# Performance work log

Measured on AMD Instinct MI355X. Metric: run time of the kernel, lower is better.

Reference implementation:

```python
import jax, jax.numpy as jnp
import numpy as np

NC = 6            # CPAB tessellation cells (tess_size=6, zero_boundary=True)
DIM = NC - 1      # theta dimension = 5
SIG_LEN = 2048
CHANNELS = 3
BATCH = 256
FC_IN = 64 * 168  # flattened net_part1 output for signal_len=2048
NUM_SCALING = 0   # N in transform_data_ss
EPS_BN = 1e-5


def _cpab_basis():
    """QR null-space basis of the CPAB continuity + zero-boundary constraints.
    Params ordered [a_1,b_1,...,a_NC,b_NC]; v(x)=a_c x + b_c on cell c."""
    nc = NC
    L = np.zeros((nc + 1, 2 * nc))
    for k in range(1, nc):  # continuity at internal knots x_k = k/nc
        xk = k / nc
        L[k - 1, 2 * (k - 1)] = xk
        L[k - 1, 2 * (k - 1) + 1] = 1.0
        L[k - 1, 2 * k] = -xk
        L[k - 1, 2 * k + 1] = -1.0
    L[nc - 1, 1] = 1.0        # v(0) = 0  -> b_1 = 0
    L[nc, 2 * (nc - 1)] = 1.0  # v(1) = 0 -> a_nc + b_nc = 0
    L[nc, 2 * nc - 1] = 1.0
    Q, _ = np.linalg.qr(L.T, mode='complete')
    return np.ascontiguousarray(Q[:, nc + 1:]).astype(np.float32)  # (12, 5)


def _conv1d(x, w, b):
    y = jax.lax.conv_general_dilated(x, w, (1,), 'VALID',
                                     dimension_numbers=('NCH', 'OIH', 'NCH'))
    return y + b[None, :, None]


def _maxpool1d(x, k, s):
    return jax.lax.reduce_window(x, -jnp.inf, jax.lax.max, (1, 1, k), (1, 1, s), 'VALID')


def _bn(x, g, b, m, v):  # eval-mode BatchNorm1d
    return (x - m[None, :, None]) * (g / jnp.sqrt(v + EPS_BN))[None, :, None] + b[None, :, None]


def _integrate(x, A):
    """Exact CPAB 1D flow integration over t=1 with cell-crossing handling.
    x: (B, n) points in [0,1]; A: (B, NC, 2) per-cell (a, b). Monotone
    trajectories cross at most NC-1 boundaries -> fixed NC+1 iterations."""
    a_all, b_all = A[:, :, 0], A[:, :, 1]
    t = jnp.ones_like(x)
    for _ in range(NC + 1):
        c = jnp.clip(jnp.floor(x * NC).astype(jnp.int32), 0, NC - 1)
        a = jnp.take_along_axis(a_all, c, axis=1)
        b = jnp.take_along_axis(b_all, c, axis=1)
        v = a * x + b
        xb = jnp.where(v >= 0, (c + 1).astype(x.dtype) / NC, c.astype(x.dtype) / NC)
        big_a = jnp.abs(a) > 1e-8
        a_s = jnp.where(big_a, a, 1.0)
        z = x + b / a_s        # shifted coord: x(t) = z*exp(a t) - b/a
        zb = xb + b / a_s
        ratio = zb / jnp.where(jnp.abs(z) > 1e-12, z, 1e-12)
        t_exp = jnp.log(jnp.maximum(ratio, 1e-12)) / a_s
        v_s = jnp.where(jnp.abs(v) > 1e-12, v, 1.0)
        t_lin = (xb - x) / v_s
        thit = jnp.where(big_a, t_exp, t_lin)
        valid = (jnp.abs(v) > 1e-12) & (thit > 0) & (jnp.where(big_a, ratio, 1.0) > 0)
        thit = jnp.where(valid, thit, jnp.inf)
        tau = jnp.minimum(t, thit)
        x_new = jnp.where(big_a, z * jnp.exp(a * tau) - (z - x), x + b * tau)
        hit = thit <= t
        nudge = jnp.where(v >= 0, 1e-6, -1e-6)  # push into next cell
        x = jnp.clip(jnp.where(hit, xb + nudge, x_new), 0.0, 1.0)
        t = jnp.maximum(t - tau, 0.0)
    return x


def _interp1d(data, pos):
    """data: (B, L, C); pos: (B, n) in [0,1] -> (B, n, C) linear interpolation."""
    Lw = data.shape[1]
    p = jnp.clip(pos, 0.0, 1.0) * (Lw - 1)
    x0 = jnp.clip(jnp.floor(p).astype(jnp.int32), 0, Lw - 2)
    w = (p - x0.astype(p.dtype))[:, :, None]
    d0 = jnp.take_along_axis(data, x0[:, :, None], axis=1)
    d1 = jnp.take_along_axis(data, (x0 + 1)[:, :, None], axis=1)
    return d0 * (1.0 - w) + d1 * w


def _transform_data_ss(data, theta, basis, outsize, N):
    """CPAB scaling-and-squaring warp of data (B, L, C) by theta (B, DIM)."""
    Bsz = theta.shape[0]
    A = (theta @ basis.T).reshape(Bsz, NC, 2) / (2.0 ** N)
    grid = jnp.linspace(0.0, 1.0, outsize, dtype=data.dtype)
    grid_t = _integrate(jnp.broadcast_to(grid, (Bsz, outsize)), A)
    for _ in range(N):  # squaring: compose the warp with itself
        grid_t = _interp1d(grid_t[:, :, None], grid_t)[:, :, 0]
    return _interp1d(data, grid_t)


def reference(x, conv1_w, conv1_b, bn1_g, bn1_b, bn1_m, bn1_v,
              conv2_w, conv2_b, bn2_g, bn2_b, bn2_m, bn2_v,
              conv3_w, conv3_b, bn3_g, bn3_b, bn3_m, bn3_v,
              fc1_w, fc1_b, fc2_w, fc2_b, fc3_w, fc3_b, fc4_w, fc4_b, basis):
    # localization net (n_recurrence = 1, back_version = True)
    h = jax.nn.relu(_maxpool1d(_bn(_conv1d(x, conv1_w, conv1_b), bn1_g, bn1_b, bn1_m, bn1_v), 3, 2))
    h = jax.nn.relu(_maxpool1d(_bn(_conv1d(h, conv2_w, conv2_b), bn2_g, bn2_b, bn2_m, bn2_v), 3, 3))
    h = jax.nn.relu(_maxpool1d(_bn(_conv1d(h, conv3_w, conv3_b), bn3_g, bn3_b, bn3_m, bn3_v), 3, 2))
    xs = h.reshape(h.shape[0], -1)  # (B, 64*168)
    xs = jax.nn.relu(xs @ fc1_w.T + fc1_b)
    xs = jax.nn.relu(xs @ fc2_w.T + fc2_b)
    xs = jax.nn.relu(xs @ fc3_w.T + fc3_b)
    theta = jnp.tanh(xs @ fc4_w.T + fc4_b)  # (B, 5)
    data = jnp.transpose(x, (0, 2, 1))       # (B, L, C)
    warped = _transform_data_ss(data, theta, basis, SIG_LEN, NUM_SCALING)
    return jnp.transpose(warped, (0, 2, 1))  # (B, C, L)


def setup_inputs() -> dict:
    key = jax.random.key(0)
    ks = jax.random.split(key, 16)
    def nrm(k, shape, scale):
        return (jax.random.normal(k, shape) * scale).astype(jnp.float32)
    inp = {}
    inp['x'] = jax.random.normal(ks[0], (BATCH, CHANNELS, SIG_LEN), dtype=jnp.float32)
    inp['conv1_w'] = nrm(ks[1], (128, CHANNELS, 3), (CHANNELS * 3) ** -0.5)
    inp['conv1_b'] = nrm(ks[2], (128,), 0.01)
    inp['bn1_g'] = jnp.ones((128,), jnp.float32)
    inp['bn1_b'] = jnp.zeros((128,), jnp.float32)
    inp['bn1_m'] = nrm(ks[3], (128,), 0.1)
    inp['bn1_v'] = jnp.ones((128,), jnp.float32)
    inp['conv2_w'] = nrm(ks[4], (64, 128, 5), (128 * 5) ** -0.5)
    inp['conv2_b'] = nrm(ks[5], (64,), 0.01)
    inp['bn2_g'] = jnp.ones((64,), jnp.float32)
    inp['bn2_b'] = jnp.zeros((64,), jnp.float32)
    inp['bn2_m'] = nrm(ks[6], (64,), 0.1)
    inp['bn2_v'] = jnp.ones((64,), jnp.float32)
    inp['conv3_w'] = nrm(ks[7], (64, 64, 3), (64 * 3) ** -0.5)
    inp['conv3_b'] = nrm(ks[8], (64,), 0.01)
    inp['bn3_g'] = jnp.ones((64,), jnp.float32)
    inp['bn3_b'] = jnp.zeros((64,), jnp.float32)
    inp['bn3_m'] = nrm(ks[9], (64,), 0.1)
    inp['bn3_v'] = jnp.ones((64,), jnp.float32)
    inp['fc1_w'] = nrm(ks[10], (48, FC_IN), FC_IN ** -0.5)
    inp['fc1_b'] = jnp.zeros((48,), jnp.float32)
    inp['fc2_w'] = nrm(ks[11], (32, 48), 48 ** -0.5)
    inp['fc2_b'] = jnp.zeros((32,), jnp.float32)
    inp['fc3_w'] = nrm(ks[12], (16, 32), 32 ** -0.5)
    inp['fc3_b'] = jnp.zeros((16,), jnp.float32)
    # near-identity warp head (original zero-inits weight, identity bias)
    inp['fc4_w'] = nrm(ks[13], (DIM, 16), 0.01)
    inp['fc4_b'] = nrm(ks[14], (DIM,), 0.01)
    inp['basis'] = jnp.asarray(_cpab_basis())
    return inp
```

## Files before the change

kernel.cpp:

```cpp
#include <hip/hip_runtime.h>
#include <math.h>

#define BATCH   256
#define SIGLEN  2048
#define L1OUT   1022
#define L2OUT   339
#define L3OUT   168
#define FCIN    10752

#define TP2   16
#define NROW  52
#define H1S   136
#define H1SZ  (NROW*H1S)

#define TU3   28

typedef float f32x4  __attribute__((ext_vector_type(4)));
typedef short s16x8  __attribute__((ext_vector_type(8)));

__device__ __forceinline__ unsigned short f2bf(float f) {
    unsigned int u = __float_as_uint(f);
    return (unsigned short)((u + 0x7fffu + ((u >> 16) & 1u)) >> 16);
}
__device__ __forceinline__ float bf2f(unsigned short h) {
    return __uint_as_float(((unsigned int)h) << 16);
}

__launch_bounds__(256)
__global__ void prep_kernel(
    const float* __restrict__ conv1_b,
    const float* __restrict__ g1, const float* __restrict__ b1,
    const float* __restrict__ m1, const float* __restrict__ v1,
    const float* __restrict__ conv2_w, const float* __restrict__ conv2_b,
    const float* __restrict__ g2, const float* __restrict__ b2,
    const float* __restrict__ m2, const float* __restrict__ v2,
    const float* __restrict__ conv3_w, const float* __restrict__ conv3_b,
    const float* __restrict__ g3, const float* __restrict__ b3,
    const float* __restrict__ m3, const float* __restrict__ v3,
    const float* __restrict__ fc1_w,
    unsigned short* __restrict__ w2hi, unsigned short* __restrict__ w2lo,
    unsigned short* __restrict__ w3hi, unsigned short* __restrict__ w3lo,
    float* __restrict__ wp1,
    float* __restrict__ so1, float* __restrict__ so2, float* __restrict__ so3)
{
    __shared__ float tl[64 * 169];

    int t   = threadIdx.x;
    int tid = blockIdx.x * 256 + t;
    int stride = gridDim.x * 256;

    if (blockIdx.x < 48) {
        int o = blockIdx.x;
        for (int i = t; i < FCIN; i += 256) {
            int co = i / L3OUT, u = i - co * L3OUT;
            tl[co * 169 + u] = fc1_w[o * FCIN + i];
        }
        __syncthreads();
        for (int i = t; i < FCIN; i += 256) {
            int u = i >> 6, co = i & 63;
            wp1[o * FCIN + i] = tl[co * 169 + u];
        }
    }

    for (int i = tid; i < 64*128*5; i += stride) {
        int co = i / 640; int rr = i - co*640; int ci = rr / 5; int k = rr - ci*5;
        float w = conv2_w[i];
        unsigned short hi = f2bf(w);
        unsigned short lo = f2bf(w - bf2f(hi));
        int dst = ((k*4 + (ci >> 5))*64 + co)*32 + (ci & 31);
        w2hi[dst] = hi;
        w2lo[dst] = lo;
    }
    for (int i = tid; i < 64*64*3; i += stride) {
        int co = i / 192; int r = i - co*192; int ci = r / 3; int k = r - ci*3;
        float w = conv3_w[i];
        unsigned short hi = f2bf(w);
        unsigned short lo = f2bf(w - bf2f(hi));
        int dst = ((k*2 + (ci >> 5))*64 + co)*32 + (ci & 31);
        w3hi[dst] = hi;
        w3lo[dst] = lo;
    }
    if (tid < 128) {
        float s = g1[tid] / sqrtf(v1[tid] + 1e-5f);
        so1[tid]       = s;
        so1[128 + tid] = (conv1_b[tid] - m1[tid]) * s + b1[tid];
    }
    if (tid < 64) {
        float s2 = g2[tid] / sqrtf(v2[tid] + 1e-5f);
        so2[tid]      = s2;
        so2[64 + tid] = (conv2_b[tid] - m2[tid]) * s2 + b2[tid];
        float s3 = g3[tid] / sqrtf(v3[tid] + 1e-5f);
        so3[tid]      = s3;
        so3[64 + tid] = (conv3_b[tid] - m3[tid]) * s3 + b3[tid];
    }
}

__launch_bounds__(256, 5)
__global__ void conv12_kernel(
    const float* __restrict__ x, const float* __restrict__ w1,
    const unsigned short* __restrict__ w2hi, const unsigned short* __restrict__ w2lo,
    const float* __restrict__ so1, const float* __restrict__ so2,
    unsigned int* __restrict__ h2p)
{
    __shared__ unsigned short h1hi[H1SZ];
    __shared__ unsigned short h1lo[H1SZ];

    int t  = threadIdx.x;
    int b  = blockIdx.x;
    int u0 = blockIdx.y * TP2;
    int q0 = 3 * u0;
    int wv = __builtin_amdgcn_readfirstlane(t >> 6);
    int l  = t & 63;
    int m  = l & 15;
    int qd = l >> 4;

    float wr[2][9];
    float s1r[2], o1r[2];
    #pragma unroll
    for (int h = 0; h < 2; ++h) {
        int ch = l + 64*h;
        #pragma unroll
        for (int j = 0; j < 9; ++j) wr[h][j] = w1[ch*9 + j];
        s1r[h] = so1[ch]; o1r[h] = so1[128 + ch];
    }
    for (int s = 0; s < 13; ++s) {
        int r = 4*s + wv;
        int xbase = 2*(q0 + r);
        float xv[3][5];
        if (xbase + 4 <= SIGLEN - 1) {
            #pragma unroll
            for (int ci = 0; ci < 3; ++ci) {
                const float* xp = x + (b*3 + ci)*SIGLEN + xbase;
                float2 v01 = *(const float2*)(xp);
                float2 v23 = *(const float2*)(xp + 2);
                xv[ci][0] = v01.x; xv[ci][1] = v01.y;
                xv[ci][2] = v23.x; xv[ci][3] = v23.y;
                xv[ci][4] = xp[4];
            }
        } else {
            #pragma unroll
            for (int ci = 0; ci < 3; ++ci) {
                const float* xp = x + (b*3 + ci)*SIGLEN;
                #pragma unroll
                for (int d = 0; d < 5; ++d) {
                    int xi = xbase + d; xi = xi < SIGLEN ? xi : SIGLEN - 1;
                    xv[ci][d] = xp[xi];
                }
            }
        }
        #pragma unroll
        for (int h = 0; h < 2; ++h) {
            float r0 = 0.f, r1 = 0.f, r2 = 0.f;
            #pragma unroll
            for (int ci = 0; ci < 3; ++ci) {
                float wA = wr[h][ci*3], wB = wr[h][ci*3+1], wC = wr[h][ci*3+2];
                r0 = fmaf(xv[ci][0], wA, fmaf(xv[ci][1], wB, fmaf(xv[ci][2], wC, r0)));
                r1 = fmaf(xv[ci][1], wA, fmaf(xv[ci][2], wB, fmaf(xv[ci][3], wC, r1)));
                r2 = fmaf(xv[ci][2], wA, fmaf(xv[ci][3], wB, fmaf(xv[ci][4], wC, r2)));
            }
            float mx = fmaxf(r0, fmaxf(r1, r2));
            float v  = fmaxf(fmaf(s1r[h], mx, o1r[h]), 0.f);
            unsigned short hi = f2bf(v);
            unsigned short lo = f2bf(v - bf2f(hi));
            h1hi[r*H1S + l + 64*h] = hi;
            h1lo[r*H1S + l + 64*h] = lo;
        }
    }
    __syncthreads();

    f32x4 acc[3] = {(f32x4)(0.f), (f32x4)(0.f), (f32x4)(0.f)};

    const unsigned short* whb = w2hi + wv*512 + m*32 + qd*8;
    const unsigned short* wlb = w2lo + wv*512 + m*32 + qd*8;

    for (int k = 0; k < 5; ++k) {
        #pragma unroll
        for (int cb = 0; cb < 4; ++cb) {
            int st = k*4 + cb;
            s16x8 wh = *(const s16x8*)(whb + st*2048);
            s16x8 wl = *(const s16x8*)(wlb + st*2048);
            #pragma unroll
            for (int pt = 0; pt < 3; ++pt) {
                int row = pt*16 + m + k;
                s16x8 ah = *(const s16x8*)&h1hi[row*H1S + cb*32 + qd*8];
                s16x8 al = *(const s16x8*)&h1lo[row*H1S + cb*32 + qd*8];
                acc[pt] = __builtin_amdgcn_mfma_f32_16x16x32_bf16(ah, wh, acc[pt], 0, 0, 0);
                acc[pt] = __builtin_amdgcn_mfma_f32_16x16x32_bf16(al, wh, acc[pt], 0, 0, 0);
                acc[pt] = __builtin_amdgcn_mfma_f32_16x16x32_bf16(ah, wl, acc[pt], 0, 0, 0);
            }
        }
    }
    __syncthreads();

    float* c2 = (float*)h1hi;
    #pragma unroll
    for (int pt = 0; pt < 3; ++pt)
        #pragma unroll
        for (int rg = 0; rg < 4; ++rg)
            c2[(pt*16 + qd*4 + rg)*65 + wv*16 + m] = acc[pt][rg];
    __syncthreads();

    #pragma unroll
    for (int it = 0; it < 4; ++it) {
        int idx = t + it*256;
        int ul = idx >> 6, co = idx & 63;
        int u = u0 + ul;
        if (u < L2OUT) {
            float v0 = c2[(3*ul  )*65 + co];
            float v1 = c2[(3*ul+1)*65 + co];
            float v2 = c2[(3*ul+2)*65 + co];
            float mm = fmaxf(v0, fmaxf(v1, v2));
            float v  = fmaxf(fmaf(so2[co], mm, so2[64 + co]), 0.f);
            unsigned short hi = f2bf(v);
            unsigned short lo = f2bf(v - bf2f(hi));
            h2p[(b*L2OUT + u)*64 + co] = (unsigned int)hi | ((unsigned int)lo << 16);
        }
    }
}

__launch_bounds__(256, 4)
__global__ void conv3fc1_kernel(
    const unsigned int* __restrict__ h2p,
    const unsigned short* __restrict__ w3hi, const unsigned short* __restrict__ w3lo,
    const float* __restrict__ so3, const float* __restrict__ wp1,
    float* __restrict__ part)
{
    __shared__ unsigned short h3s[2*66*72];
    __shared__ float c3buf[64*65];

    int t  = threadIdx.x;
    int b  = blockIdx.x;
    int ti = blockIdx.y;
    int u0 = ti * TU3;
    int wv = __builtin_amdgcn_readfirstlane(t >> 6);
    int l  = t & 63;
    int m  = l & 15;
    int qd = l >> 4;

    for (int i = t; i < 66*64; i += 256) {
        int r = i >> 6, ci = i & 63;
        int g = 2*u0 + r; g = g > (L2OUT-1) ? (L2OUT-1) : g;
        unsigned int v = h2p[(b*L2OUT + g)*64 + ci];
        h3s[r*72 + ci]         = (unsigned short)(v & 0xffffu);
        h3s[66*72 + r*72 + ci] = (unsigned short)(v >> 16);
    }
    __syncthreads();

    s16x8 wh[6], wl[6];
    #pragma unroll
    for (int s = 0; s < 6; ++s) {
        wh[s] = *(const s16x8*)(w3hi + s*2048 + (wv*16 + m)*32 + qd*8);
        wl[s] = *(const s16x8*)(w3lo + s*2048 + (wv*16 + m)*32 + qd*8);
    }

    f32x4 acc[4] = {(f32x4)(0.f), (f32x4)(0.f), (f32x4)(0.f), (f32x4)(0.f)};
    #pragma unroll
    for (int pt = 0; pt < 4; ++pt) {
        #pragma unroll
        for (int s = 0; s < 6; ++s) {
            int row = pt*16 + m + (s >> 1);
            int off = (s & 1)*32 + qd*8;
            s16x8 ah = *(const s16x8*)&h3s[row*72 + off];
            s16x8 al = *(const s16x8*)&h3s[66*72 + row*72 + off];
            acc[pt] = __builtin_amdgcn_mfma_f32_16x16x32_bf16(ah, wh[s], acc[pt], 0, 0, 0);
            acc[pt] = __builtin_amdgcn_mfma_f32_16x16x32_bf16(al, wh[s], acc[pt], 0, 0, 0);
            acc[pt] = __builtin_amdgcn_mfma_f32_16x16x32_bf16(ah, wl[s], acc[pt], 0, 0, 0);
        }
    }
    __syncthreads();

    #pragma unroll
    for (int pt = 0; pt < 4; ++pt)
        #pragma unroll
        for (int rg = 0; rg < 4; ++rg)
            c3buf[(pt*16 + qd*4 + rg)*65 + wv*16 + m] = acc[pt][rg];
    __syncthreads();

    float s3 = so3[l], o3 = so3[64 + l];
    float pooled[TU3];
    #pragma unroll
    for (int u = 0; u < TU3; ++u) {
        int p = 2*u;
        float v0 = c3buf[(p  )*65 + l];
        float v1 = c3buf[(p+1)*65 + l];
        float v2 = c3buf[(p+2)*65 + l];
        pooled[u] = fmaxf(fmaf(s3, fmaxf(v0, fmaxf(v1, v2)), o3), 0.f);
    }

    int o0 = wv * 12;
    float fa[12];
    #pragma unroll
    for (int j = 0; j < 12; ++j) fa[j] = 0.f;
    #pragma unroll 4
    for (int u = 0; u < TU3; ++u) {
        float pv = pooled[u];
        const float* wp = wp1 + (u0 + u)*64 + l;
        #pragma unroll
        for (int j = 0; j < 12; ++j)
            fa[j] = fmaf(pv, wp[(o0 + j)*FCIN], fa[j]);
    }
    #pragma unroll
    for (int j = 0; j < 12; ++j) {
        #pragma unroll
        for (int off = 32; off > 0; off >>= 1)
            fa[j] += __shfl_xor(fa[j], off, 64);
    }
    if (l == 0) {
        #pragma unroll
        for (int j = 0; j < 12; ++j)
            part[(b*6 + ti)*48 + o0 + j] = fa[j];
    }
}

__launch_bounds__(256)
__global__ void warp_kernel(
    const float* __restrict__ x, const float* __restrict__ part,
    const float* __restrict__ fc1_b,
    const float* __restrict__ fc2_w, const float* __restrict__ fc2_b,
    const float* __restrict__ fc3_w, const float* __restrict__ fc3_b,
    const float* __restrict__ fc4_w, const float* __restrict__ fc4_b,
    const float* __restrict__ basis,
    float* __restrict__ out)
{
    __shared__ float xs48[48], hl[32], gl[16], thl[5], Al[12];

    int b = blockIdx.x;
    int t = threadIdx.x;

    if (t < 48) {
        float sv = 0.f;
        #pragma unroll
        for (int ti = 0; ti < 6; ++ti) sv += part[(b*6 + ti)*48 + t];
        xs48[t] = fmaxf(sv + fc1_b[t], 0.f);
    }
    __syncthreads();
    if (t < 32) {
        float sv = fc2_b[t];
        #pragma unroll
        for (int k = 0; k < 48; ++k) sv = fmaf(fc2_w[t * 48 + k], xs48[k], sv);
        hl[t] = fmaxf(sv, 0.f);
    }
    __syncthreads();
    if (t < 16) {
        float sv = fc3_b[t];
        #pragma unroll
        for (int k = 0; k < 32; ++k) sv = fmaf(fc3_w[t * 32 + k], hl[k], sv);
        gl[t] = fmaxf(sv, 0.f);
    }
    __syncthreads();
    if (t < 5) {
        float sv = fc4_b[t];
        #pragma unroll
        for (int k = 0; k < 16; ++k) sv = fmaf(fc4_w[t * 16 + k], gl[k], sv);
        thl[t] = tanhf(sv);
    }
    __syncthreads();
    if (t < 12) {
        float sv = 0.f;
        #pragma unroll
        for (int d = 0; d < 5; ++d) sv = fmaf(basis[t * 5 + d], thl[d], sv);
        Al[t] = sv;
    }
    __syncthreads();

    float a_r[6], b_r[6];
    #pragma unroll
    for (int c = 0; c < 6; ++c) { a_r[c] = Al[2*c]; b_r[c] = Al[2*c+1]; }

    #pragma unroll
    for (int cc = 0; cc < 2; ++cc) {
        int i = (blockIdx.y * 2 + cc) * 256 + t;
        float xp = (float)i / 2047.f;
        float tt = 1.f;
        for (int it = 0; it < 7; ++it) {
            int c = (int)floorf(xp * 6.f);
            c = min(max(c, 0), 5);
            float a  = a_r[c], bb = b_r[c];
            float v  = a * xp + bb;
            float xb = (v >= 0.f) ? (float)(c + 1) / 6.f : (float)c / 6.f;
            bool  big_a = fabsf(a) > 1e-8f;
            float a_s = big_a ? a : 1.f;
            float z   = xp + bb / a_s;
            float zb  = xb + bb / a_s;
            float zden = (fabsf(z) > 1e-12f) ? z : 1e-12f;
            float ratio = zb / zden;
            float t_exp = logf(fmaxf(ratio, 1e-12f)) / a_s;
            float v_s   = (fabsf(v) > 1e-12f) ? v : 1.f;
            float t_lin = (xb - xp) / v_s;
            float thit  = big_a ? t_exp : t_lin;
            bool valid  = (fabsf(v) > 1e-12f) && (thit > 0.f) && ((big_a ? ratio : 1.f) > 0.f);
            if (!valid) thit = __builtin_inff();
            float tau   = fminf(tt, thit);
            float x_new = big_a ? (z * expf(a * tau) - (z - xp)) : (xp + bb * tau);
            bool hit    = (thit <= tt);
            float nudge = (v >= 0.f) ? 1e-6f : -1e-6f;
            xp = hit ? (xb + nudge) : x_new;
            xp = fminf(fmaxf(xp, 0.f), 1.f);
            tt = fmaxf(tt - tau, 0.f);
        }
        float p = fminf(fmaxf(xp, 0.f), 1.f) * 2047.f;
        int i0 = (int)floorf(p);
        i0 = min(max(i0, 0), 2046);
        float w = p - (float)i0;
        #pragma unroll
        for (int c = 0; c < 3; ++c) {
            const float* d = &x[(b * 3 + c) * SIGLEN];
            out[(b * 3 + c) * SIGLEN + i] = d[i0] * (1.f - w) + d[i0 + 1] * w;
        }
    }
}

extern "C" void kernel_launch(void* const* d_in, const int* in_sizes, int n_in,
                              void* d_out, int out_size, void* d_ws, size_t ws_size,
                              hipStream_t stream) {
    (void)in_sizes; (void)n_in; (void)out_size; (void)ws_size;
    const float* x       = (const float*)d_in[0];
    const float* conv1_w = (const float*)d_in[1];
    const float* conv1_b = (const float*)d_in[2];
    const float* bn1_g   = (const float*)d_in[3];
    const float* bn1_b   = (const float*)d_in[4];
    const float* bn1_m   = (const float*)d_in[5];
    const float* bn1_v   = (const float*)d_in[6];
    const float* conv2_w = (const float*)d_in[7];
    const float* conv2_b = (const float*)d_in[8];
    const float* bn2_g   = (const float*)d_in[9];
    const float* bn2_b   = (const float*)d_in[10];
    const float* bn2_m   = (const float*)d_in[11];
    const float* bn2_v   = (const float*)d_in[12];
    const float* conv3_w = (const float*)d_in[13];
    const float* conv3_b = (const float*)d_in[14];
    const float* bn3_g   = (const float*)d_in[15];
    const float* bn3_b   = (const float*)d_in[16];
    const float* bn3_m   = (const float*)d_in[17];
    const float* bn3_v   = (const float*)d_in[18];
    const float* fc1_w   = (const float*)d_in[19];
    const float* fc1_b   = (const float*)d_in[20];
    const float* fc2_w   = (const float*)d_in[21];
    const float* fc2_b   = (const float*)d_in[22];
    const float* fc3_w   = (const float*)d_in[23];
    const float* fc3_b   = (const float*)d_in[24];
    const float* fc4_w   = (const float*)d_in[25];
    const float* fc4_b   = (const float*)d_in[26];
    const float* basis   = (const float*)d_in[27];

    unsigned short* w2hi = (unsigned short*)d_ws;
    unsigned short* w2lo = w2hi + 40960;
    unsigned short* w3hi = w2lo + 40960;
    unsigned short* w3lo = w3hi + 12288;
    float* ws   = (float*)d_ws;
    float* so1  = ws + 53248;
    float* so2  = so1 + 256;
    float* so3  = so2 + 128;
    float* wp1  = so3 + 128;
    unsigned int* h2p = (unsigned int*)(wp1 + 516096);
    float* part = (float*)(h2p + 5554176);

    prep_kernel<<<128, 256, 0, stream>>>(
        conv1_b, bn1_g, bn1_b, bn1_m, bn1_v,
        conv2_w, conv2_b, bn2_g, bn2_b, bn2_m, bn2_v,
        conv3_w, conv3_b, bn3_g, bn3_b, bn3_m, bn3_v,
        fc1_w, w2hi, w2lo, w3hi, w3lo, wp1, so1, so2, so3);

    dim3 g2(BATCH, (L2OUT + TP2 - 1) / TP2);
    conv12_kernel<<<g2, 256, 0, stream>>>(x, conv1_w, w2hi, w2lo, so1, so2, h2p);

    dim3 g3(BATCH, 6);
    conv3fc1_kernel<<<g3, 256, 0, stream>>>(h2p, w3hi, w3lo, so3, wp1, part);

    dim3 g5(BATCH, 4);
    warp_kernel<<<g5, 256, 0, stream>>>(x, part, fc1_b, fc2_w, fc2_b,
                                        fc3_w, fc3_b, fc4_w, fc4_b, basis,
                                        (float*)d_out);
}
```

Baseline: 247.4 us.

## Restructure conv12 with 32x32 MFMA tiles, larger blocks, swizzled LDS and sliding-window conv1

Doubles the conv2 output tile per block to 32 pooled positions with 512 threads, and switches the conv2 GEMM from 16x16x32 to 32x32x16 bf16 MFMA with a matching weight layout. The block has 8 waves but only 6 run MFMA tiles, and which waves sit idle rotates with the block index. Conv1 now uses a per-wave sliding window that reuses the overlapping window result and loads only two new inputs per row. h1 is stored as packed channel pairs with an XOR swizzle to avoid LDS bank conflicts. The bf16 hi/lo split now uses truncation instead of round-to-nearest, which changes rounding slightly. The larger tile wastes some rows at the sequence tail, and the bigger LDS footprint may reduce occupancy.

After: 250.0 us. About the same (+1.0%).

```diff
diff --git a/kernel.cpp b/kernel.cpp
--- a/kernel.cpp
+++ b/kernel.cpp
@@ -8,15 +8,15 @@
 #define L3OUT   168
 #define FCIN    10752
 
-#define TP2   16
-#define NROW  52
-#define H1S   136
-#define H1SZ  (NROW*H1S)
+#define TP2   32
+#define NROW  100
+#define PLANE (NROW*128)
 
 #define TU3   28
 
-typedef float f32x4  __attribute__((ext_vector_type(4)));
-typedef short s16x8  __attribute__((ext_vector_type(8)));
+typedef float f32x4   __attribute__((ext_vector_type(4)));
+typedef float f32x16  __attribute__((ext_vector_type(16)));
+typedef short s16x8   __attribute__((ext_vector_type(8)));
 
 __device__ __forceinline__ unsigned short f2bf(float f) {
     unsigned int u = __float_as_uint(f);
@@ -67,7 +67,7 @@
         float w = conv2_w[i];
         unsigned short hi = f2bf(w);
         unsigned short lo = f2bf(w - bf2f(hi));
-        int dst = ((k*4 + (ci >> 5))*64 + co)*32 + (ci & 31);
+        int dst = ((k*8 + (ci >> 4))*64 + co)*16 + (ci & 15);
         w2hi[dst] = hi;
         w2lo[dst] = lo;
     }
@@ -95,114 +95,172 @@
     }
 }
 
-__launch_bounds__(256, 5)
+__launch_bounds__(512, 6)
 __global__ void conv12_kernel(
     const float* __restrict__ x, const float* __restrict__ w1,
     const unsigned short* __restrict__ w2hi, const unsigned short* __restrict__ w2lo,
     const float* __restrict__ so1, const float* __restrict__ so2,
     unsigned int* __restrict__ h2p)
 {
-    __shared__ unsigned short h1hi[H1SZ];
-    __shared__ unsigned short h1lo[H1SZ];
+    __shared__ unsigned short h1[2*PLANE];
+    unsigned short* h1hi = h1;
+    unsigned short* h1lo = h1 + PLANE;
 
     int t  = threadIdx.x;
     int b  = blockIdx.x;
-    int u0 = blockIdx.y * TP2;
-    int q0 = 3 * u0;
+    int by = blockIdx.y;
+    int u0 = by * TP2;
     int wv = __builtin_amdgcn_readfirstlane(t >> 6);
     int l  = t & 63;
-    int m  = l & 15;
-    int qd = l >> 4;
-
-    float wr[2][9];
-    float s1r[2], o1r[2];
-    #pragma unroll
-    for (int h = 0; h < 2; ++h) {
-        int ch = l + 64*h;
-        #pragma unroll
-        for (int j = 0; j < 9; ++j) wr[h][j] = w1[ch*9 + j];
-        s1r[h] = so1[ch]; o1r[h] = so1[128 + ch];
-    }
-    for (int s = 0; s < 13; ++s) {
-        int r = 4*s + wv;
-        int xbase = 2*(q0 + r);
-        float xv[3][5];
-        if (xbase + 4 <= SIGLEN - 1) {
+
+    {
+        float wr[2][9], s1r[2], o1r[2];
+        #pragma unroll
+        for (int h = 0; h < 2; ++h) {
+            int ch = 2*l + h;
+            #pragma unroll
+            for (int j = 0; j < 9; ++j) wr[h][j] = w1[ch*9 + j];
+            s1r[h] = so1[ch]; o1r[h] = so1[128 + ch];
+        }
+
+        int rbase = 13 * wv;
+        int W0 = 192*by + 2*rbase;
+        const float* xp0 = x + b*3*SIGLEN;
+
+        float xv[3][6];
+        if (W0 + 5 <= SIGLEN - 1) {
             #pragma unroll
             for (int ci = 0; ci < 3; ++ci) {
-                const float* xp = x + (b*3 + ci)*SIGLEN + xbase;
+                const float* xp = xp0 + ci*SIGLEN + W0;
                 float2 v01 = *(const float2*)(xp);
                 float2 v23 = *(const float2*)(xp + 2);
+                float2 v45 = *(const float2*)(xp + 4);
                 xv[ci][0] = v01.x; xv[ci][1] = v01.y;
                 xv[ci][2] = v23.x; xv[ci][3] = v23.y;
-                xv[ci][4] = xp[4];
+                xv[ci][4] = v45.x; xv[ci][5] = v45.y;
             }
         } else {
             #pragma unroll
-            for (int ci = 0; ci < 3; ++ci) {
-                const float* xp = x + (b*3 + ci)*SIGLEN;
+            for (int ci = 0; ci < 3; ++ci)
                 #pragma unroll
-                for (int d = 0; d < 5; ++d) {
-                    int xi = xbase + d; xi = xi < SIGLEN ? xi : SIGLEN - 1;
-                    xv[ci][d] = xp[xi];
+                for (int j = 0; j < 6; ++j) {
+                    int xi = W0 + j; xi = xi < SIGLEN ? xi : SIGLEN - 1;
+                    xv[ci][j] = xp0[ci*SIGLEN + xi];
+                }
+        }
+
+        float cr0 = 0.f, cr1 = 0.f;
+        #pragma unroll
+        for (int s = 0; s < 13; ++s) {
+            int r = rbase + s;
+            if (r < NROW) {
+                float vo[2];
+                #pragma unroll
+                for (int h = 0; h < 2; ++h) {
+                    float r0, r1 = 0.f, r2 = 0.f;
+                    if (s == 0) {
+                        r0 = 0.f;
+                        #pragma unroll
+                        for (int ci = 0; ci < 3; ++ci)
+                            r0 = fmaf(xv[ci][0], wr[h][ci*3],
+                                 fmaf(xv[ci][1], wr[h][ci*3+1],
+                                 fmaf(xv[ci][2], wr[h][ci*3+2], r0)));
+                    } else {
+                        r0 = h ? cr1 : cr0;
+                    }
+                    #pragma unroll
+                    for (int ci = 0; ci < 3; ++ci) {
+                        float wA = wr[h][ci*3], wB = wr[h][ci*3+1], wC = wr[h][ci*3+2];
+                        r1 = fmaf(xv[ci][1], wA, fmaf(xv[ci][2], wB, fmaf(xv[ci][3], wC, r1)));
+                        r2 = fmaf(xv[ci][2], wA, fmaf(xv[ci][3], wB, fmaf(xv[ci][4], wC, r2)));
+                    }
+                    if (h) cr1 = r2; else cr0 = r2;
+                    float mx = fmaxf(r0, fmaxf(r1, r2));
+                    vo[h] = fmaxf(fmaf(s1r[h], mx, o1r[h]), 0.f);
+                }
+                unsigned ua = __float_as_uint(vo[0]);
+                unsigned ub = __float_as_uint(vo[1]);
+                unsigned hb = ub & 0xffff0000u;
+                unsigned hipack = (ua >> 16) | hb;
+                float ra = vo[0] - __uint_as_float(ua & 0xffff0000u);
+                float rb = vo[1] - __uint_as_float(hb);
+                unsigned lopack = (__float_as_uint(ra) >> 16) | (__float_as_uint(rb) & 0xffff0000u);
+                int wi = r*64 + (l ^ ((r & 7) << 2));
+                ((unsigned*)h1hi)[wi] = hipack;
+                ((unsigned*)h1lo)[wi] = lopack;
+            }
+            if (s < 12) {
+                #pragma unroll
+                for (int ci = 0; ci < 3; ++ci) {
+                    xv[ci][0] = xv[ci][2]; xv[ci][1] = xv[ci][3];
+                    xv[ci][2] = xv[ci][4]; xv[ci][3] = xv[ci][5];
+                }
+                int Wn = W0 + 2*s + 6;
+                if (Wn + 1 <= SIGLEN - 1) {
+                    #pragma unroll
+                    for (int ci = 0; ci < 3; ++ci) {
+                        float2 v = *(const float2*)(xp0 + ci*SIGLEN + Wn);
+                        xv[ci][4] = v.x; xv[ci][5] = v.y;
+                    }
+                } else {
+                    #pragma unroll
+                    for (int ci = 0; ci < 3; ++ci) {
+                        int x4 = Wn     < SIGLEN ? Wn     : SIGLEN - 1;
+                        int x5 = Wn + 1 < SIGLEN ? Wn + 1 : SIGLEN - 1;
+                        xv[ci][4] = xp0[ci*SIGLEN + x4];
+                        xv[ci][5] = xp0[ci*SIGLEN + x5];
+                    }
                 }
             }
         }
-        #pragma unroll
-        for (int h = 0; h < 2; ++h) {
-            float r0 = 0.f, r1 = 0.f, r2 = 0.f;
+    }
+    __syncthreads();
+
+    int tid8 = (wv + ((b + by) & 7)) & 7;
+    int active = tid8 < 6;
+    int mt = tid8 >> 1;
+    int nt = tid8 & 1;
+    int lm  = l & 31;
+    int hi8 = (l >> 5) * 8;
+
+    f32x16 acc = (f32x16)(0.f);
+    if (active) {
+        const unsigned short* wbh = w2hi + (nt*32 + lm)*16 + hi8;
+        const unsigned short* wbl = w2lo + (nt*32 + lm)*16 + hi8;
+        #pragma unroll
+        for (int k = 0; k < 5; ++k) {
+            int row = mt*32 + lm + k;
+            int sb  = row*128 + hi8;
+            int swz = (row & 7) << 3;
             #pragma unroll
-            for (int ci = 0; ci < 3; ++ci) {
-                float wA = wr[h][ci*3], wB = wr[h][ci*3+1], wC = wr[h][ci*3+2];
-                r0 = fmaf(xv[ci][0], wA, fmaf(xv[ci][1], wB, fmaf(xv[ci][2], wC, r0)));
-                r1 = fmaf(xv[ci][1], wA, fmaf(xv[ci][2], wB, fmaf(xv[ci][3], wC, r1)));
-                r2 = fmaf(xv[ci][2], wA, fmaf(xv[ci][3], wB, fmaf(xv[ci][4], wC, r2)));
+            for (int c16 = 0; c16 < 8; ++c16) {
+                int st = k*8 + c16;
+                s16x8 wh = *(const s16x8*)(wbh + st*1024);
+                s16x8 wl = *(const s16x8*)(wbl + st*1024);
+                int idx = (sb + c16*16) ^ swz;
+                s16x8 ah = *(const s16x8*)&h1hi[idx];
+                s16x8 al = *(const s16x8*)&h1lo[idx];
+                acc = __builtin_amdgcn_mfma_f32_32x32x16_bf16(ah, wh, acc, 0, 0, 0);
+                acc = __builtin_amdgcn_mfma_f32_32x32x16_bf16(al, wh, acc, 0, 0, 0);
+                acc = __builtin_amdgcn_mfma_f32_32x32x16_bf16(ah, wl, acc, 0, 0, 0);
             }
-            float mx = fmaxf(r0, fmaxf(r1, r2));
-            float v  = fmaxf(fmaf(s1r[h], mx, o1r[h]), 0.f);
-            unsigned short hi = f2bf(v);
-            unsigned short lo = f2bf(v - bf2f(hi));
-            h1hi[r*H1S + l + 64*h] = hi;
-            h1lo[r*H1S + l + 64*h] = lo;
-        }
-    }
-    __syncthreads();
-
-    f32x4 acc[3] = {(f32x4)(0.f), (f32x4)(0.f), (f32x4)(0.f)};
-
-    const unsigned short* whb = w2hi + wv*512 + m*32 + qd*8;
-    const unsigned short* wlb = w2lo + wv*512 + m*32 + qd*8;
-
-    for (int k = 0; k < 5; ++k) {
-        #pragma unroll
-        for (int cb = 0; cb < 4; ++cb) {
-            int st = k*4 + cb;
-            s16x8 wh = *(const s16x8*)(whb + st*2048);
-            s16x8 wl = *(const s16x8*)(wlb + st*2048);
-            #pragma unroll
-            for (int pt = 0; pt < 3; ++pt) {
-                int row = pt*16 + m + k;
-                s16x8 ah = *(const s16x8*)&h1hi[row*H1S + cb*32 + qd*8];
-                s16x8 al = *(const s16x8*)&h1lo[row*H1S + cb*32 + qd*8];
-                acc[pt] = __builtin_amdgcn_mfma_f32_16x16x32_bf16(ah, wh, acc[pt], 0, 0, 0);
-                acc[pt] = __builtin_amdgcn_mfma_f32_16x16x32_bf16(al, wh, acc[pt], 0, 0, 0);
-                acc[pt] = __builtin_amdgcn_mfma_f32_16x16x32_bf16(ah, wl, acc[pt], 0, 0, 0);
-            }
-        }
-    }
-    __syncthreads();
-
-    float* c2 = (float*)h1hi;
-    #pragma unroll
-    for (int pt = 0; pt < 3; ++pt)
-        #pragma unroll
-        for (int rg = 0; rg < 4; ++rg)
-            c2[(pt*16 + qd*4 + rg)*65 + wv*16 + m] = acc[pt][rg];
+        }
+    }
+    __syncthreads();
+
+    float* c2 = (float*)h1;
+    if (active) {
+        #pragma unroll
+        for (int rg = 0; rg < 16; ++rg) {
+            int prow = mt*32 + (rg & 3) + 8*(rg >> 2) + 4*(l >> 5);
+            c2[prow*65 + nt*32 + lm] = acc[rg];
+        }
+    }
     __syncthreads();
 
     #pragma unroll
     for (int it = 0; it < 4; ++it) {
-        int idx = t + it*256;
+        int idx = t + it*512;
         int ul = idx >> 6, co = idx & 63;
         int u = u0 + ul;
         if (u < L2OUT) {
@@ -211,9 +269,9 @@
             float v2 = c2[(3*ul+2)*65 + co];
             float mm = fmaxf(v0, fmaxf(v1, v2));
             float v  = fmaxf(fmaf(so2[co], mm, so2[64 + co]), 0.f);
-            unsigned short hi = f2bf(v);
-            unsigned short lo = f2bf(v - bf2f(hi));
-            h2p[(b*L2OUT + u)*64 + co] = (unsigned int)hi | ((unsigned int)lo << 16);
+            unsigned uu = __float_as_uint(v);
+            float rr = v - __uint_as_float(uu & 0xffff0000u);
+            h2p[(b*L2OUT + u)*64 + co] = (uu >> 16) | (__float_as_uint(rr) & 0xffff0000u);
         }
     }
 }
@@ -462,7 +520,7 @@
         fc1_w, w2hi, w2lo, w3hi, w3lo, wp1, so1, so2, so3);
 
     dim3 g2(BATCH, (L2OUT + TP2 - 1) / TP2);
-    conv12_kernel<<<g2, 256, 0, stream>>>(x, conv1_w, w2hi, w2lo, so1, so2, h2p);
+    conv12_kernel<<<g2, 512, 0, stream>>>(x, conv1_w, w2hi, w2lo, so1, so2, h2p);
 
     dim3 g3(BATCH, 6);
     conv3fc1_kernel<<<g3, 256, 0, stream>>>(h2p, w3hi, w3lo, so3, wp1, part);
```

## Restructure conv1 stage with packed FMAs, sliding window reuse, truncated bf16 split

Applied to the files above, without the earlier changes.

The conv1+pool stage is reorganised so each thread computes two adjacent channels with packed v_pk_fma_f32 instructions. Each wave now handles a contiguous block of 13 rows and slides an input window, reusing the overlapping conv output between consecutive pooled rows instead of recomputing it. The bf16 hi/lo split is changed from round-to-nearest to truncation with byte-permute packing, which cuts ALU work but changes rounding (hi+lo still approximates the value closely). The aim is to reduce VALU and load work in the conv12 kernel's first phase. The risks are more register pressure and slightly different numerics.

Result: faster. 242.2 us (-2.1%).

```diff
diff --git a/kernel.cpp b/kernel.cpp
--- a/kernel.cpp
+++ b/kernel.cpp
@@ -15,6 +15,7 @@
 
 #define TU3   28
 
+typedef float f32x2  __attribute__((ext_vector_type(2)));
 typedef float f32x4  __attribute__((ext_vector_type(4)));
 typedef short s16x8  __attribute__((ext_vector_type(8)));
 
@@ -24,6 +25,11 @@
 }
 __device__ __forceinline__ float bf2f(unsigned short h) {
     return __uint_as_float(((unsigned int)h) << 16);
+}
+__device__ __forceinline__ f32x2 pkfma(f32x2 a, f32x2 b, f32x2 c) {
+    f32x2 d;
+    asm("v_pk_fma_f32 %0, %1, %2, %3" : "=v"(d) : "v"(a), "v"(b), "v"(c));
+    return d;
 }
 
 __launch_bounds__(256)
@@ -114,56 +120,111 @@
     int m  = l & 15;
     int qd = l >> 4;
 
-    float wr[2][9];
-    float s1r[2], o1r[2];
-    #pragma unroll
-    for (int h = 0; h < 2; ++h) {
-        int ch = l + 64*h;
-        #pragma unroll
-        for (int j = 0; j < 9; ++j) wr[h][j] = w1[ch*9 + j];
-        s1r[h] = so1[ch]; o1r[h] = so1[128 + ch];
-    }
-    for (int s = 0; s < 13; ++s) {
-        int r = 4*s + wv;
-        int xbase = 2*(q0 + r);
-        float xv[3][5];
-        if (xbase + 4 <= SIGLEN - 1) {
+    {
+        f32x2 wp[9], s1p, o1p;
+        const float* wa = w1 + (2*l)*9;
+        #pragma unroll
+        for (int j = 0; j < 9; ++j) wp[j] = (f32x2){wa[j], wa[9 + j]};
+        s1p = (f32x2){so1[2*l], so1[2*l + 1]};
+        o1p = (f32x2){so1[128 + 2*l], so1[128 + 2*l + 1]};
+
+        int rbase = 13 * wv;
+        int W0 = 2*(q0 + rbase);
+        const float* xp0 = x + b*3*SIGLEN;
+
+        f32x2 xb[3][6];
+        if (W0 + 5 <= SIGLEN - 1) {
             #pragma unroll
             for (int ci = 0; ci < 3; ++ci) {
-                const float* xp = x + (b*3 + ci)*SIGLEN + xbase;
+                const float* xp = xp0 + ci*SIGLEN + W0;
                 float2 v01 = *(const float2*)(xp);
                 float2 v23 = *(const float2*)(xp + 2);
-                xv[ci][0] = v01.x; xv[ci][1] = v01.y;
-                xv[ci][2] = v23.x; xv[ci][3] = v23.y;
-                xv[ci][4] = xp[4];
+                float2 v45 = *(const float2*)(xp + 4);
+                xb[ci][0] = (f32x2){v01.x, v01.x};
+                xb[ci][1] = (f32x2){v01.y, v01.y};
+                xb[ci][2] = (f32x2){v23.x, v23.x};
+                xb[ci][3] = (f32x2){v23.y, v23.y};
+                xb[ci][4] = (f32x2){v45.x, v45.x};
+                xb[ci][5] = (f32x2){v45.y, v45.y};
             }
         } else {
             #pragma unroll
+            for (int ci = 0; ci < 3; ++ci)
+                #pragma unroll
+                for (int j = 0; j < 6; ++j) {
+                    int xi = W0 + j; xi = xi < SIGLEN ? xi : SIGLEN - 1;
+                    float v = xp0[ci*SIGLEN + xi];
+                    xb[ci][j] = (f32x2){v, v};
+                }
+        }
+
+        f32x2 cr = (f32x2){0.f, 0.f};
+        #pragma unroll
+        for (int s = 0; s < 13; ++s) {
+            int r = rbase + s;
+            f32x2 r1 = (f32x2){0.f, 0.f}, r2 = (f32x2){0.f, 0.f};
+            #pragma unroll
             for (int ci = 0; ci < 3; ++ci) {
-                const float* xp = x + (b*3 + ci)*SIGLEN;
                 #pragma unroll
-                for (int d = 0; d < 5; ++d) {
-                    int xi = xbase + d; xi = xi < SIGLEN ? xi : SIGLEN - 1;
-                    xv[ci][d] = xp[xi];
+                for (int tp = 0; tp < 3; ++tp) {
+                    r1 = pkfma(xb[ci][1 + tp], wp[ci*3 + tp], r1);
+                    r2 = pkfma(xb[ci][2 + tp], wp[ci*3 + tp], r2);
                 }
             }
-        }
-        #pragma unroll
-        for (int h = 0; h < 2; ++h) {
-            float r0 = 0.f, r1 = 0.f, r2 = 0.f;
-            #pragma unroll
-            for (int ci = 0; ci < 3; ++ci) {
-                float wA = wr[h][ci*3], wB = wr[h][ci*3+1], wC = wr[h][ci*3+2];
-                r0 = fmaf(xv[ci][0], wA, fmaf(xv[ci][1], wB, fmaf(xv[ci][2], wC, r0)));
-                r1 = fmaf(xv[ci][1], wA, fmaf(xv[ci][2], wB, fmaf(xv[ci][3], wC, r1)));
-                r2 = fmaf(xv[ci][2], wA, fmaf(xv[ci][3], wB, fmaf(xv[ci][4], wC, r2)));
+            f32x2 r0;
+            if (s == 0) {
+                r0 = (f32x2){0.f, 0.f};
+                #pragma unroll
+                for (int ci = 0; ci < 3; ++ci)
+                    #pragma unroll
+                    for (int tp = 0; tp < 3; ++tp)
+                        r0 = pkfma(xb[ci][tp], wp[ci*3 + tp], r0);
+            } else {
+                r0 = cr;
             }
-            float mx = fmaxf(r0, fmaxf(r1, r2));
-            float v  = fmaxf(fmaf(s1r[h], mx, o1r[h]), 0.f);
-            unsigned short hi = f2bf(v);
-            unsigned short lo = f2bf(v - bf2f(hi));
-            h1hi[r*H1S + l + 64*h] = hi;
-            h1lo[r*H1S + l + 64*h] = lo;
+            cr = r2;
+
+            float m0 = fmaxf(r0[0], fmaxf(r1[0], r2[0]));
+            float m1 = fmaxf(r0[1], fmaxf(r1[1], r2[1]));
+            float v0 = fmaxf(fmaf(s1p[0], m0, o1p[0]), 0.f);
+            float v1 = fmaxf(fmaf(s1p[1], m1, o1p[1]), 0.f);
+
+            unsigned ua = __float_as_uint(v0);
+            unsigned ub = __float_as_uint(v1);
+            unsigned hipack = __builtin_amdgcn_perm(ub, ua, 0x07060302u);
+            float ra = v0 - __uint_as_float(ua & 0xffff0000u);
+            float rb = v1 - __uint_as_float(ub & 0xffff0000u);
+            unsigned lopack = __builtin_amdgcn_perm(__float_as_uint(rb), __float_as_uint(ra),
+                                                    0x07060302u);
+            ((unsigned*)h1hi)[r*68 + l] = hipack;
+            ((unsigned*)h1lo)[r*68 + l] = lopack;
+
+            if (s < 12) {
+                #pragma unroll
+                for (int ci = 0; ci < 3; ++ci) {
+                    xb[ci][0] = xb[ci][2]; xb[ci][1] = xb[ci][3];
+                    xb[ci][2] = xb[ci][4]; xb[ci][3] = xb[ci][5];
+                }
+                int Wn = W0 + 2*s + 6;
+                if (Wn + 1 <= SIGLEN - 1) {
+                    #pragma unroll
+                    for (int ci = 0; ci < 3; ++ci) {
+                        float2 v = *(const float2*)(xp0 + ci*SIGLEN + Wn);
+                        xb[ci][4] = (f32x2){v.x, v.x};
+                        xb[ci][5] = (f32x2){v.y, v.y};
+                    }
+                } else {
+                    #pragma unroll
+                    for (int ci = 0; ci < 3; ++ci) {
+                        int x4 = Wn     < SIGLEN ? Wn     : SIGLEN - 1;
+                        int x5 = Wn + 1 < SIGLEN ? Wn + 1 : SIGLEN - 1;
+                        float a4 = xp0[ci*SIGLEN + x4];
+                        float a5 = xp0[ci*SIGLEN + x5];
+                        xb[ci][4] = (f32x2){a4, a4};
+                        xb[ci][5] = (f32x2){a5, a5};
+                    }
+                }
+            }
         }
     }
     __syncthreads();
@@ -211,9 +272,9 @@
             float v2 = c2[(3*ul+2)*65 + co];
             float mm = fmaxf(v0, fmaxf(v1, v2));
             float v  = fmaxf(fmaf(so2[co], mm, so2[64 + co]), 0.f);
-            unsigned short hi = f2bf(v);
-            unsigned short lo = f2bf(v - bf2f(hi));
-            h2p[(b*L2OUT + u)*64 + co] = (unsigned int)hi | ((unsigned int)lo << 16);
+            unsigned uu = __float_as_uint(v);
+            float rr = v - __uint_as_float(uu & 0xffff0000u);
+            h2p[(b*L2OUT + u)*64 + co] = (uu >> 16) | (__float_as_uint(rr) & 0xffff0000u);
         }
     }
 }
```
